# Optimization experiments

Hardware: AMD Instinct MI355X
Metric: run time of the kernel (lower is better)

Reference implementation:

```python
import jax, jax.numpy as jnp
import numpy as np

B, S, DIM, H = 8, 2048, 128, 8
HD = DIM // H  # 16
SCALE = 1.0 / np.sqrt(256.0).astype(np.float32)  # faithful: original divides by sqrt(256)=16


def setup_inputs() -> dict:
    key = jax.random.key(0)
    ks = jax.random.split(key, 8)
    w_std = 1.0 / np.sqrt(DIM).astype(np.float32)
    return {
        "q": jax.random.normal(ks[0], (B, S, DIM), jnp.float32),
        "k": jax.random.normal(ks[1], (B, S, DIM), jnp.float32),
        "v": jax.random.normal(ks[2], (B, S, DIM), jnp.float32),
        "Wq": jax.random.normal(ks[3], (DIM, DIM), jnp.float32) * w_std,
        "bq": jnp.zeros((DIM,), jnp.float32),
        "Wk": jax.random.normal(ks[4], (DIM, DIM), jnp.float32) * w_std,
        "bk": jnp.zeros((DIM,), jnp.float32),
        "Wv": jax.random.normal(ks[5], (DIM, DIM), jnp.float32) * w_std,
        "bv": jnp.zeros((DIM,), jnp.float32),
        "Wo": jax.random.normal(ks[6], (DIM, DIM), jnp.float32) * w_std,
        "bo": jnp.zeros((DIM,), jnp.float32),
    }


def reference(q, k, v, Wq, bq, Wk, bk, Wv, bv, Wo, bo):
    # QKV projections
    Q = q @ Wq + bq  # [B,S,DIM]
    K = k @ Wk + bk
    V = v @ Wv + bv
    # split heads: [B,H,S,HD]
    Q = Q.reshape(B, S, H, HD).transpose(0, 2, 1, 3)
    K = K.reshape(B, S, H, HD).transpose(0, 2, 1, 3)
    V = V.reshape(B, S, H, HD).transpose(0, 2, 1, 3)
    # scaled dot-product attention (note non-standard scale 1/16)
    scores = jnp.einsum("bhqd,bhkd->bhqk", Q, K) * SCALE
    attn = jax.nn.softmax(scores, axis=-1)
    out = jnp.einsum("bhqk,bhkd->bhqd", attn, V)
    out = out.transpose(0, 2, 1, 3).reshape(B, S, DIM)
    return out @ Wo + bo
```

## Files before the change

### kernel.cpp

```cpp
#include <hip/hip_runtime.h>

typedef __attribute__((ext_vector_type(8))) short short8;
typedef __attribute__((ext_vector_type(16))) float f32x16;
typedef _Float16 h8 __attribute__((ext_vector_type(8)));
typedef unsigned int uint;
typedef unsigned short ushort;

#define NS 2048
#define QSCALE 0.0901684400555602f

__device__ __forceinline__ ushort f2h(float f) {
  _Float16 h = (_Float16)f;
  return __builtin_bit_cast(ushort, h);
}
__device__ __forceinline__ uint pkrtz_u(float a, float b) {
  uint r;
  asm("v_cvt_pkrtz_f16_f32 %0, %1, %2" : "=v"(r) : "v"(a), "v"(b));
  return r;
}
__device__ __forceinline__ float fast_exp2(float x) {
#if __has_builtin(__builtin_amdgcn_exp2f)
  return __builtin_amdgcn_exp2f(x);
#else
  return exp2f(x);
#endif
}

__global__ __launch_bounds__(256) void qkv_mfma(
    const float* __restrict__ qin, const float* __restrict__ kin, const float* __restrict__ vin,
    const float* __restrict__ Wq, const float* __restrict__ bq,
    const float* __restrict__ Wk, const float* __restrict__ bk,
    const float* __restrict__ Wv, const float* __restrict__ bv,
    ushort* __restrict__ Qh, ushort* __restrict__ Kh, ushort* __restrict__ Vt) {
  __shared__ __align__(16) ushort Wt[128 * 136];
  __shared__ __align__(16) ushort Al[64 * 136];
  const int tid = threadIdx.x;
  const int p = blockIdx.y;
  const float* A = (p == 0) ? qin : (p == 1) ? kin : vin;
  const float* W = (p == 0) ? Wq : (p == 1) ? Wk : Wv;
  const float* bias = (p == 0) ? bq : (p == 1) ? bk : bv;
  const float wscale = (p == 0) ? QSCALE : 1.0f;
  const int rbase = blockIdx.x * 64;
  {
    const int n = tid & 127, kg = tid >> 7;
#pragma unroll
    for (int k8 = 0; k8 < 8; ++k8) {
      int k0 = k8 * 16 + kg * 8;
      float w[8];
#pragma unroll
      for (int j = 0; j < 8; ++j) w[j] = W[(k0 + j) * 128 + n] * wscale;
      uint4 pk;
      pk.x = pkrtz_u(w[0], w[1]);
      pk.y = pkrtz_u(w[2], w[3]);
      pk.z = pkrtz_u(w[4], w[5]);
      pk.w = pkrtz_u(w[6], w[7]);
      *reinterpret_cast<uint4*>(&Wt[n * 136 + k0]) = pk;
    }
  }
#pragma unroll
  for (int it = 0; it < 8; ++it) {
    int fl = it * 256 + tid;
    int r = fl >> 5, c4 = (fl & 31) << 2;
    float4 a = *reinterpret_cast<const float4*>(A + (size_t)(rbase + r) * 128 + c4);
    uint2 pk;
    pk.x = pkrtz_u(a.x, a.y);
    pk.y = pkrtz_u(a.z, a.w);
    *reinterpret_cast<uint2*>(&Al[r * 136 + c4]) = pk;
  }
  __syncthreads();
  const int lane = tid & 63, wid = tid >> 6;
  const int l31 = lane & 31, hi = lane >> 5;
  const int rh = wid >> 1, ch = wid & 1;
  f32x16 acc[2];
#pragma unroll
  for (int i = 0; i < 2; ++i)
#pragma unroll
    for (int j = 0; j < 16; ++j) acc[i][j] = 0.f;
  const ushort* arow = &Al[(rh * 32 + l31) * 136 + hi * 8];
#pragma unroll
  for (int kk = 0; kk < 8; ++kk) {
    const h8 af = *reinterpret_cast<const h8*>(arow + kk * 16);
#pragma unroll
    for (int i = 0; i < 2; ++i) {
      int nt = ch * 2 + i;
      const h8 bf = *reinterpret_cast<const h8*>(&Wt[(nt * 32 + l31) * 136 + kk * 16 + hi * 8]);
      acc[i] = __builtin_amdgcn_mfma_f32_32x32x16_f16(af, bf, acc[i], 0, 0, 0);
    }
  }
  const int bI = rbase >> 11;
  if (p < 2) {
    ushort* outp = (p == 0) ? Qh : Kh;
#pragma unroll
    for (int i = 0; i < 2; ++i) {
      int c = (ch * 2 + i) * 32 + l31;
      int h = c >> 4, d = c & 15;
      float bb = bias[c] * wscale;
#pragma unroll
      for (int r = 0; r < 16; ++r) {
        int s = rbase + rh * 32 + ((r & 3) + ((r >> 2) << 3) + (hi << 2));
        int sl = s & 2047;
        outp[((size_t)((bI << 3) + h) * 2048 + sl) * 16 + d] = f2h(acc[i][r] + bb);
      }
    }
  } else {
    __syncthreads();
    ushort* CL = Wt;
#pragma unroll
    for (int i = 0; i < 2; ++i) {
      int c = (ch * 2 + i) * 32 + l31;
      float bb = bias[c];
#pragma unroll
      for (int g = 0; g < 4; ++g) {
        uint2 pk;
        pk.x = pkrtz_u(acc[i][g * 4 + 0] + bb, acc[i][g * 4 + 1] + bb);
        pk.y = pkrtz_u(acc[i][g * 4 + 2] + bb, acc[i][g * 4 + 3] + bb);
        int sl0 = rh * 32 + g * 8 + (hi << 2);
        *reinterpret_cast<uint2*>(&CL[c * 72 + sl0]) = pk;
      }
    }
    __syncthreads();
    const int slb = rbase & 2047;
#pragma unroll
    for (int it = 0; it < 4; ++it) {
      int fl = it * 256 + tid;
      int c = fl >> 3, s8 = (fl & 7) * 8;
      short8 val = *reinterpret_cast<const short8*>(&CL[c * 72 + s8]);
      int h = c >> 4, d = c & 15;
      *reinterpret_cast<short8*>(&Vt[((size_t)((bI << 3) + h) * 16 + d) * 2048 + slb + s8]) = val;
    }
  }
}

__global__ __launch_bounds__(256, 4) void attn_kernel(
    const ushort* __restrict__ Qh, const ushort* __restrict__ Kh,
    const ushort* __restrict__ Vtg, ushort* __restrict__ aout) {
  __shared__ __align__(16) ushort Kl[256 * 24];
  __shared__ __align__(16) ushort Vl[17 * 264];
  const int tid = threadIdx.x;
  const int lane = tid & 63, wv = tid >> 6;
  const int l31 = lane & 31, hi = lane >> 5;
  const int bh = blockIdx.x, qt = blockIdx.y;
  for (int e = tid; e < 264; e += 256) Vl[16 * 264 + e] = 0x3C00;
  const int q0 = qt * 128 + wv * 32;
  const h8 qf = *reinterpret_cast<const h8*>(Qh + ((size_t)bh * NS + q0 + l31) * 16 + hi * 8);
  f32x16 oac0, oac1, zc;
#pragma unroll
  for (int i = 0; i < 16; ++i) { oac0[i] = 0.f; oac1[i] = 0.f; zc[i] = 0.f; }
  const int vrow = (l31 < 17) ? l31 : 16;
  const ushort* Kg = Kh + (size_t)bh * NS * 16;
  const ushort* Vg = Vtg + (size_t)bh * 16 * NS;
  const ushort* kbl = &Kl[l31 * 24 + hi * 8];
  const ushort* vbase = &Vl[vrow * 264 + hi * 8];
  const int key0 = tid >> 1, hh = tid & 1, vd = tid >> 5, vc = (tid & 31) * 8;
  const int vgrp = vc & ~31, vk0 = vc & 31;
  const int vs1 = vgrp + ((vk0 & 16) | ((vk0 & 8) >> 1));

  short8 rk0, rk1, rv0, rv1;
#define LOADT(T)                                                                          \
  {                                                                                       \
    int kb = (T) * 256;                                                                   \
    rk0 = *reinterpret_cast<const short8*>(Kg + (size_t)(kb + key0) * 16 + hh * 8);       \
    rk1 = *reinterpret_cast<const short8*>(Kg + (size_t)(kb + 128 + key0) * 16 + hh * 8); \
    rv0 = *reinterpret_cast<const short8*>(Vg + (size_t)vd * NS + kb + vc);               \
    rv1 = *reinterpret_cast<const short8*>(Vg + (size_t)(8 + vd) * NS + kb + vc);         \
  }
#define WRITET()                                                                          \
  {                                                                                       \
    *reinterpret_cast<short8*>(&Kl[key0 * 24 + hh * 8]) = rk0;                            \
    *reinterpret_cast<short8*>(&Kl[(128 + key0) * 24 + hh * 8]) = rk1;                    \
    union { short8 s; uint2 u[2]; } c0, c1;                                               \
    c0.s = rv0; c1.s = rv1;                                                               \
    *reinterpret_cast<uint2*>(&Vl[vd * 264 + vs1]) = c0.u[0];                             \
    *reinterpret_cast<uint2*>(&Vl[vd * 264 + vs1 + 8]) = c0.u[1];                         \
    *reinterpret_cast<uint2*>(&Vl[(8 + vd) * 264 + vs1]) = c1.u[0];                       \
    *reinterpret_cast<uint2*>(&Vl[(8 + vd) * 264 + vs1 + 8]) = c1.u[1];                   \
  }

  LOADT(0);
  WRITET();
  __syncthreads();
  for (int t = 0; t < 8; ++t) {
    if (t < 7) LOADT(t + 1);
#pragma unroll
    for (int kt = 0; kt < 8; ++kt) {
      const h8 kf = *reinterpret_cast<const h8*>(kbl + kt * 768);
      f32x16 sc = __builtin_amdgcn_mfma_f32_32x32x16_f16(kf, qf, zc, 0, 0, 0);
      float pr[16];
#pragma unroll
      for (int r = 0; r < 16; ++r) pr[r] = fast_exp2(sc[r]);
      {
        union { uint u[4]; h8 h; } pf;
        pf.u[0] = pkrtz_u(pr[0], pr[1]);
        pf.u[1] = pkrtz_u(pr[2], pr[3]);
        pf.u[2] = pkrtz_u(pr[4], pr[5]);
        pf.u[3] = pkrtz_u(pr[6], pr[7]);
        const h8 vf = *reinterpret_cast<const h8*>(vbase + kt * 32);
        oac0 = __builtin_amdgcn_mfma_f32_32x32x16_f16(pf.h, vf, oac0, 0, 0, 0);
      }
      {
        union { uint u[4]; h8 h; } pf;
        pf.u[0] = pkrtz_u(pr[8], pr[9]);
        pf.u[1] = pkrtz_u(pr[10], pr[11]);
        pf.u[2] = pkrtz_u(pr[12], pr[13]);
        pf.u[3] = pkrtz_u(pr[14], pr[15]);
        const h8 vf = *reinterpret_cast<const h8*>(vbase + kt * 32 + 16);
        oac1 = __builtin_amdgcn_mfma_f32_32x32x16_f16(pf.h, vf, oac1, 0, 0, 0);
      }
    }
    if (t < 7) {
      __syncthreads();
      WRITET();
      __syncthreads();
    }
  }
#undef LOADT
#undef WRITET
  const int b = bh >> 3, h = bh & 7;
  const int d = l31;
#pragma unroll
  for (int r = 0; r < 16; ++r) {
    float ov = oac0[r] + oac1[r];
    float ls = __shfl(ov, 16 + (hi << 5), 64);
    if (d < 16) {
      int qrow = q0 + ((r & 3) + ((r >> 2) << 3) + (hi << 2));
      aout[((size_t)(b * NS + qrow)) * 128 + h * 16 + d] = f2h(ov / ls);
    }
  }
}

__global__ __launch_bounds__(256) void out_mfma(
    const ushort* __restrict__ Ain, const float* __restrict__ Wo,
    const float* __restrict__ bo, float* __restrict__ out) {
  __shared__ __align__(16) ushort Wt[128 * 136];
  __shared__ __align__(16) ushort Al[32 * 136];
  const int tid = threadIdx.x;
  const int rbase = blockIdx.x * 32;
  {
    const int n = tid & 127, kg = tid >> 7;
#pragma unroll
    for (int k8 = 0; k8 < 8; ++k8) {
      int k0 = k8 * 16 + kg * 8;
      float w[8];
#pragma unroll
      for (int j = 0; j < 8; ++j) w[j] = Wo[(k0 + j) * 128 + n];
      uint4 pk;
      pk.x = pkrtz_u(w[0], w[1]);
      pk.y = pkrtz_u(w[2], w[3]);
      pk.z = pkrtz_u(w[4], w[5]);
      pk.w = pkrtz_u(w[6], w[7]);
      *reinterpret_cast<uint4*>(&Wt[n * 136 + k0]) = pk;
    }
  }
#pragma unroll
  for (int it = 0; it < 2; ++it) {
    int fl = it * 256 + tid;
    int r = fl >> 4, c8 = (fl & 15) * 8;
    *reinterpret_cast<short8*>(&Al[r * 136 + c8]) =
        *reinterpret_cast<const short8*>(Ain + (size_t)(rbase + r) * 128 + c8);
  }
  __syncthreads();
  const int lane = tid & 63, wid = tid >> 6;
  const int l31 = lane & 31, hi = lane >> 5;
  f32x16 acc;
#pragma unroll
  for (int j = 0; j < 16; ++j) acc[j] = 0.f;
  const ushort* arow = &Al[l31 * 136 + hi * 8];
#pragma unroll
  for (int kk = 0; kk < 8; ++kk) {
    const h8 af = *reinterpret_cast<const h8*>(arow + kk * 16);
    const h8 bf = *reinterpret_cast<const h8*>(&Wt[(wid * 32 + l31) * 136 + kk * 16 + hi * 8]);
    acc = __builtin_amdgcn_mfma_f32_32x32x16_f16(af, bf, acc, 0, 0, 0);
  }
  const int c = wid * 32 + l31;
  const float bb = bo[c];
#pragma unroll
  for (int r = 0; r < 16; ++r) {
    int s = rbase + ((r & 3) + ((r >> 2) << 3) + (hi << 2));
    out[(size_t)s * 128 + c] = acc[r] + bb;
  }
}

extern "C" void kernel_launch(void* const* d_in, const int* in_sizes, int n_in,
                              void* d_out, int out_size, void* d_ws, size_t ws_size,
                              hipStream_t stream) {
  const float* q  = (const float*)d_in[0];
  const float* k  = (const float*)d_in[1];
  const float* v  = (const float*)d_in[2];
  const float* Wq = (const float*)d_in[3];
  const float* bq = (const float*)d_in[4];
  const float* Wk = (const float*)d_in[5];
  const float* bk = (const float*)d_in[6];
  const float* Wv = (const float*)d_in[7];
  const float* bv = (const float*)d_in[8];
  const float* Wo = (const float*)d_in[9];
  const float* bo = (const float*)d_in[10];
  float* out = (float*)d_out;

  ushort* Qh = (ushort*)d_out;
  ushort* Kh = Qh + 2097152;
  ushort* Vt = (ushort*)d_ws;
  ushort* aout = Vt + 2097152;

  hipLaunchKernelGGL(qkv_mfma, dim3(256, 3), dim3(256), 0, stream,
                     q, k, v, Wq, bq, Wk, bk, Wv, bv, Qh, Kh, Vt);
  hipLaunchKernelGGL(attn_kernel, dim3(64, 16), dim3(256), 0, stream, Qh, Kh, Vt, aout);
  hipLaunchKernelGGL(out_mfma, dim3(512), dim3(256), 0, stream, aout, Wo, bo, out);
}
```

Baseline: 57.59 us.

## Load K and V fragments directly from global memory, dropping LDS staging

The attention kernel no longer stages K and V tiles through shared memory with double-buffered register prefetch and barriers. Each lane now reads its MFMA operand fragments straight from global memory (relying on L1/L2 caching), and the ones-column used for the softmax denominator is built by a per-lane select instead of an LDS row. This removes the LDS writes and __syncthreads, but global load latency is now exposed inside the compute loop with no explicit prefetch, and the V reads are narrow 8-byte loads.

```diff
diff --git a/kernel.cpp b/kernel.cpp
--- a/kernel.cpp
+++ b/kernel.cpp
@@ -134,87 +134,60 @@
 __global__ __launch_bounds__(256, 4) void attn_kernel(
     const ushort* __restrict__ Qh, const ushort* __restrict__ Kh,
     const ushort* __restrict__ Vtg, ushort* __restrict__ aout) {
-  __shared__ __align__(16) ushort Kl[256 * 24];
-  __shared__ __align__(16) ushort Vl[17 * 264];
   const int tid = threadIdx.x;
   const int lane = tid & 63, wv = tid >> 6;
   const int l31 = lane & 31, hi = lane >> 5;
   const int bh = blockIdx.x, qt = blockIdx.y;
-  for (int e = tid; e < 264; e += 256) Vl[16 * 264 + e] = 0x3C00;
   const int q0 = qt * 128 + wv * 32;
   const h8 qf = *reinterpret_cast<const h8*>(Qh + ((size_t)bh * NS + q0 + l31) * 16 + hi * 8);
   f32x16 oac0, oac1, zc;
 #pragma unroll
   for (int i = 0; i < 16; ++i) { oac0[i] = 0.f; oac1[i] = 0.f; zc[i] = 0.f; }
-  const int vrow = (l31 < 17) ? l31 : 16;
-  const ushort* Kg = Kh + (size_t)bh * NS * 16;
-  const ushort* Vg = Vtg + (size_t)bh * 16 * NS;
-  const ushort* kbl = &Kl[l31 * 24 + hi * 8];
-  const ushort* vbase = &Vl[vrow * 264 + hi * 8];
-  const int key0 = tid >> 1, hh = tid & 1, vd = tid >> 5, vc = (tid & 31) * 8;
-  const int vgrp = vc & ~31, vk0 = vc & 31;
-  const int vs1 = vgrp + ((vk0 & 16) | ((vk0 & 8) >> 1));
-
-  short8 rk0, rk1, rv0, rv1;
-#define LOADT(T)                                                                          \
-  {                                                                                       \
-    int kb = (T) * 256;                                                                   \
-    rk0 = *reinterpret_cast<const short8*>(Kg + (size_t)(kb + key0) * 16 + hh * 8);       \
-    rk1 = *reinterpret_cast<const short8*>(Kg + (size_t)(kb + 128 + key0) * 16 + hh * 8); \
-    rv0 = *reinterpret_cast<const short8*>(Vg + (size_t)vd * NS + kb + vc);               \
-    rv1 = *reinterpret_cast<const short8*>(Vg + (size_t)(8 + vd) * NS + kb + vc);         \
-  }
-#define WRITET()                                                                          \
-  {                                                                                       \
-    *reinterpret_cast<short8*>(&Kl[key0 * 24 + hh * 8]) = rk0;                            \
-    *reinterpret_cast<short8*>(&Kl[(128 + key0) * 24 + hh * 8]) = rk1;                    \
-    union { short8 s; uint2 u[2]; } c0, c1;                                               \
-    c0.s = rv0; c1.s = rv1;                                                               \
-    *reinterpret_cast<uint2*>(&Vl[vd * 264 + vs1]) = c0.u[0];                             \
-    *reinterpret_cast<uint2*>(&Vl[vd * 264 + vs1 + 8]) = c0.u[1];                         \
-    *reinterpret_cast<uint2*>(&Vl[(8 + vd) * 264 + vs1]) = c1.u[0];                       \
-    *reinterpret_cast<uint2*>(&Vl[(8 + vd) * 264 + vs1 + 8]) = c1.u[1];                   \
-  }
-
-  LOADT(0);
-  WRITET();
-  __syncthreads();
-  for (int t = 0; t < 8; ++t) {
-    if (t < 7) LOADT(t + 1);
-#pragma unroll
-    for (int kt = 0; kt < 8; ++kt) {
-      const h8 kf = *reinterpret_cast<const h8*>(kbl + kt * 768);
-      f32x16 sc = __builtin_amdgcn_mfma_f32_32x32x16_f16(kf, qf, zc, 0, 0, 0);
-      float pr[16];
-#pragma unroll
-      for (int r = 0; r < 16; ++r) pr[r] = fast_exp2(sc[r]);
-      {
-        union { uint u[4]; h8 h; } pf;
-        pf.u[0] = pkrtz_u(pr[0], pr[1]);
-        pf.u[1] = pkrtz_u(pr[2], pr[3]);
-        pf.u[2] = pkrtz_u(pr[4], pr[5]);
-        pf.u[3] = pkrtz_u(pr[6], pr[7]);
-        const h8 vf = *reinterpret_cast<const h8*>(vbase + kt * 32);
-        oac0 = __builtin_amdgcn_mfma_f32_32x32x16_f16(pf.h, vf, oac0, 0, 0, 0);
-      }
-      {
-        union { uint u[4]; h8 h; } pf;
-        pf.u[0] = pkrtz_u(pr[8], pr[9]);
-        pf.u[1] = pkrtz_u(pr[10], pr[11]);
-        pf.u[2] = pkrtz_u(pr[12], pr[13]);
-        pf.u[3] = pkrtz_u(pr[14], pr[15]);
-        const h8 vf = *reinterpret_cast<const h8*>(vbase + kt * 32 + 16);
-        oac1 = __builtin_amdgcn_mfma_f32_32x32x16_f16(pf.h, vf, oac1, 0, 0, 0);
-      }
-    }
-    if (t < 7) {
-      __syncthreads();
-      WRITET();
-      __syncthreads();
-    }
-  }
-#undef LOADT
-#undef WRITET
+  const int vrow = (l31 < 16) ? l31 : 0;
+  const bool vones = (l31 >= 16);
+  const uint ONES2 = 0x3C003C00u;
+  const ushort* kp = Kh + (size_t)bh * NS * 16 + l31 * 16 + hi * 8;
+  const ushort* Vr = Vtg + (size_t)bh * 16 * NS + (size_t)vrow * NS + hi * 4;
+
+#pragma unroll 4
+  for (int c = 0; c < 64; ++c) {
+    const int kb = c * 32;
+    const h8 kf = *reinterpret_cast<const h8*>(kp + (size_t)kb * 16);
+    f32x16 sc = __builtin_amdgcn_mfma_f32_32x32x16_f16(kf, qf, zc, 0, 0, 0);
+    float pr[16];
+#pragma unroll
+    for (int r = 0; r < 16; ++r) pr[r] = fast_exp2(sc[r]);
+    {
+      union { uint u[4]; h8 h; } pf;
+      pf.u[0] = pkrtz_u(pr[0], pr[1]);
+      pf.u[1] = pkrtz_u(pr[2], pr[3]);
+      pf.u[2] = pkrtz_u(pr[4], pr[5]);
+      pf.u[3] = pkrtz_u(pr[6], pr[7]);
+      const uint2 va = *reinterpret_cast<const uint2*>(Vr + kb);
+      const uint2 vb = *reinterpret_cast<const uint2*>(Vr + kb + 8);
+      union { uint u[4]; h8 h; } vv;
+      vv.u[0] = vones ? ONES2 : va.x;
+      vv.u[1] = vones ? ONES2 : va.y;
+      vv.u[2] = vones ? ONES2 : vb.x;
+      vv.u[3] = vones ? ONES2 : vb.y;
+      oac0 = __builtin_amdgcn_mfma_f32_32x32x16_f16(pf.h, vv.h, oac0, 0, 0, 0);
+    }
+    {
+      union { uint u[4]; h8 h; } pf;
+      pf.u[0] = pkrtz_u(pr[8], pr[9]);
+      pf.u[1] = pkrtz_u(pr[10], pr[11]);
+      pf.u[2] = pkrtz_u(pr[12], pr[13]);
+      pf.u[3] = pkrtz_u(pr[14], pr[15]);
+      const uint2 va = *reinterpret_cast<const uint2*>(Vr + kb + 16);
+      const uint2 vb = *reinterpret_cast<const uint2*>(Vr + kb + 24);
+      union { uint u[4]; h8 h; } vv;
+      vv.u[0] = vones ? ONES2 : va.x;
+      vv.u[1] = vones ? ONES2 : va.y;
+      vv.u[2] = vones ? ONES2 : vb.x;
+      vv.u[3] = vones ? ONES2 : vb.y;
+      oac1 = __builtin_amdgcn_mfma_f32_32x32x16_f16(pf.h, vv.h, oac1, 0, 0, 0);
+    }
+  }
   const int b = bh >> 3, h = bh & 7;
   const int d = l31;
 #pragma unroll
```

New measurement: 103.5 us. +79.8%, slower.

## Split attention over key range with a separate combine kernel

Applied to the files above, without the earlier changes.

Adds a split-K attention kernel that processes half the keys per block (grid z=2), writing unnormalized fp16 partial outputs and row sums to workspace, plus a combine kernel that adds the partials and normalizes before the output projection. This doubles the number of attention blocks to fill more CUs and shortens each block's serial key loop. In exchange it adds an extra kernel launch and extra global traffic for the partials. It falls back to the original path if the workspace is too small. There is no max subtraction, so the sum of the two partials stays consistent.

```diff
diff --git a/kernel.cpp b/kernel.cpp
--- a/kernel.cpp
+++ b/kernel.cpp
@@ -213,8 +213,6 @@
       __syncthreads();
     }
   }
-#undef LOADT
-#undef WRITET
   const int b = bh >> 3, h = bh & 7;
   const int d = l31;
 #pragma unroll
@@ -226,6 +224,128 @@
       aout[((size_t)(b * NS + qrow)) * 128 + h * 16 + d] = f2h(ov / ls);
     }
   }
+#undef LOADT
+#undef WRITET
+}
+
+__global__ __launch_bounds__(256, 4) void attn_split(
+    const ushort* __restrict__ Qh, const ushort* __restrict__ Kh,
+    const ushort* __restrict__ Vtg, ushort* __restrict__ po, float* __restrict__ ps) {
+  __shared__ __align__(16) ushort Kl[256 * 24];
+  __shared__ __align__(16) ushort Vl[17 * 264];
+  const int tid = threadIdx.x;
+  const int lane = tid & 63, wv = tid >> 6;
+  const int l31 = lane & 31, hi = lane >> 5;
+  const int bh = blockIdx.x, qt = blockIdx.y, split = blockIdx.z;
+  const int koff = split * 1024;
+  for (int e = tid; e < 264; e += 256) Vl[16 * 264 + e] = 0x3C00;
+  const int q0 = qt * 128 + wv * 32;
+  const h8 qf = *reinterpret_cast<const h8*>(Qh + ((size_t)bh * NS + q0 + l31) * 16 + hi * 8);
+  f32x16 oac0, oac1, zc;
+#pragma unroll
+  for (int i = 0; i < 16; ++i) { oac0[i] = 0.f; oac1[i] = 0.f; zc[i] = 0.f; }
+  const int vrow = (l31 < 17) ? l31 : 16;
+  const ushort* Kg = Kh + (size_t)bh * NS * 16;
+  const ushort* Vg = Vtg + (size_t)bh * 16 * NS;
+  const ushort* kbl = &Kl[l31 * 24 + hi * 8];
+  const ushort* vbase = &Vl[vrow * 264 + hi * 8];
+  const int key0 = tid >> 1, hh = tid & 1, vd = tid >> 5, vc = (tid & 31) * 8;
+  const int vgrp = vc & ~31, vk0 = vc & 31;
+  const int vs1 = vgrp + ((vk0 & 16) | ((vk0 & 8) >> 1));
+
+  short8 rk0, rk1, rv0, rv1;
+#define LOADT(T)                                                                          \
+  {                                                                                       \
+    int kb = koff + (T) * 256;                                                            \
+    rk0 = *reinterpret_cast<const short8*>(Kg + (size_t)(kb + key0) * 16 + hh * 8);       \
+    rk1 = *reinterpret_cast<const short8*>(Kg + (size_t)(kb + 128 + key0) * 16 + hh * 8); \
+    rv0 = *reinterpret_cast<const short8*>(Vg + (size_t)vd * NS + kb + vc);               \
+    rv1 = *reinterpret_cast<const short8*>(Vg + (size_t)(8 + vd) * NS + kb + vc);         \
+  }
+#define WRITET()                                                                          \
+  {                                                                                       \
+    *reinterpret_cast<short8*>(&Kl[key0 * 24 + hh * 8]) = rk0;                            \
+    *reinterpret_cast<short8*>(&Kl[(128 + key0) * 24 + hh * 8]) = rk1;                    \
+    union { short8 s; uint2 u[2]; } c0, c1;                                               \
+    c0.s = rv0; c1.s = rv1;                                                               \
+    *reinterpret_cast<uint2*>(&Vl[vd * 264 + vs1]) = c0.u[0];                             \
+    *reinterpret_cast<uint2*>(&Vl[vd * 264 + vs1 + 8]) = c0.u[1];                         \
+    *reinterpret_cast<uint2*>(&Vl[(8 + vd) * 264 + vs1]) = c1.u[0];                       \
+    *reinterpret_cast<uint2*>(&Vl[(8 + vd) * 264 + vs1 + 8]) = c1.u[1];                   \
+  }
+
+  LOADT(0);
+  WRITET();
+  __syncthreads();
+  for (int t = 0; t < 4; ++t) {
+    if (t < 3) LOADT(t + 1);
+#pragma unroll
+    for (int kt = 0; kt < 8; ++kt) {
+      const h8 kf = *reinterpret_cast<const h8*>(kbl + kt * 768);
+      f32x16 sc = __builtin_amdgcn_mfma_f32_32x32x16_f16(kf, qf, zc, 0, 0, 0);
+      float pr[16];
+#pragma unroll
+      for (int r = 0; r < 16; ++r) pr[r] = fast_exp2(sc[r]);
+      {
+        union { uint u[4]; h8 h; } pf;
+        pf.u[0] = pkrtz_u(pr[0], pr[1]);
+        pf.u[1] = pkrtz_u(pr[2], pr[3]);
+        pf.u[2] = pkrtz_u(pr[4], pr[5]);
+        pf.u[3] = pkrtz_u(pr[6], pr[7]);
+        const h8 vf = *reinterpret_cast<const h8*>(vbase + kt * 32);
+        oac0 = __builtin_amdgcn_mfma_f32_32x32x16_f16(pf.h, vf, oac0, 0, 0, 0);
+      }
+      {
+        union { uint u[4]; h8 h; } pf;
+        pf.u[0] = pkrtz_u(pr[8], pr[9]);
+        pf.u[1] = pkrtz_u(pr[10], pr[11]);
+        pf.u[2] = pkrtz_u(pr[12], pr[13]);
+        pf.u[3] = pkrtz_u(pr[14], pr[15]);
+        const h8 vf = *reinterpret_cast<const h8*>(vbase + kt * 32 + 16);
+        oac1 = __builtin_amdgcn_mfma_f32_32x32x16_f16(pf.h, vf, oac1, 0, 0, 0);
+      }
+    }
+    if (t < 3) {
+      __syncthreads();
+      WRITET();
+      __syncthreads();
+    }
+  }
+#undef LOADT
+#undef WRITET
+  const int d = l31;
+  const size_t base = (size_t)(split * 64 + bh) * 2048;
+#pragma unroll
+  for (int r = 0; r < 16; ++r) {
+    float ov = oac0[r] + oac1[r];
+    float ls = __shfl(ov, 16 + (hi << 5), 64);
+    int qrow = q0 + ((r & 3) + ((r >> 2) << 3) + (hi << 2));
+    if (d < 16) po[(base + qrow) * 16 + d] = f2h(ov);
+    if (d == 0) ps[base + qrow] = ls;
+  }
+}
+
+__global__ __launch_bounds__(256) void combine_kernel(
+    const ushort* __restrict__ po, const float* __restrict__ ps,
+    ushort* __restrict__ aout) {
+  const int i8 = blockIdx.x * 256 + threadIdx.x;
+  const int flat = i8 * 8;
+  const int d0 = flat & 15;
+  const int qrow = (flat >> 4) & 2047;
+  const int bh = flat >> 15;
+  const h8 a = *reinterpret_cast<const h8*>(po + flat);
+  const h8 b = *reinterpret_cast<const h8*>(po + 2097152 + flat);
+  const float s = ps[bh * 2048 + qrow] + ps[131072 + bh * 2048 + qrow];
+  const float rinv = 1.0f / s;
+  union { uint u[4]; short8 s8; } o;
+#pragma unroll
+  for (int j = 0; j < 4; ++j) {
+    float v0 = ((float)a[2 * j] + (float)b[2 * j]) * rinv;
+    float v1 = ((float)a[2 * j + 1] + (float)b[2 * j + 1]) * rinv;
+    o.u[j] = pkrtz_u(v0, v1);
+  }
+  const size_t idx = ((size_t)((bh >> 3) * 2048 + qrow)) * 128 + (bh & 7) * 16 + d0;
+  *reinterpret_cast<short8*>(aout + idx) = o.s8;
 }
 
 __global__ __launch_bounds__(256) void out_mfma(
@@ -299,10 +419,21 @@
   ushort* Qh = (ushort*)d_out;
   ushort* Kh = Qh + 2097152;
   ushort* Vt = (ushort*)d_ws;
-  ushort* aout = Vt + 2097152;
 
   hipLaunchKernelGGL(qkv_mfma, dim3(256, 3), dim3(256), 0, stream,
                      q, k, v, Wq, bq, Wk, bk, Wv, bv, Qh, Kh, Vt);
-  hipLaunchKernelGGL(attn_kernel, dim3(64, 16), dim3(256), 0, stream, Qh, Kh, Vt, aout);
-  hipLaunchKernelGGL(out_mfma, dim3(512), dim3(256), 0, stream, aout, Wo, bo, out);
-}
+
+  if (ws_size >= 13631488u) {
+    ushort* po = Vt + 2097152;
+    float* ps = (float*)((char*)d_ws + 12582912);
+    ushort* aout = Vt;
+    hipLaunchKernelGGL(attn_split, dim3(64, 16, 2), dim3(256), 0, stream,
+                       Qh, Kh, Vt, po, ps);
+    hipLaunchKernelGGL(combine_kernel, dim3(1024), dim3(256), 0, stream, po, ps, aout);
+    hipLaunchKernelGGL(out_mfma, dim3(512), dim3(256), 0, stream, aout, Wo, bo, out);
+  } else {
+    ushort* aout = Vt + 2097152;
+    hipLaunchKernelGGL(attn_kernel, dim3(64, 16), dim3(256), 0, stream, Qh, Kh, Vt, aout);
+    hipLaunchKernelGGL(out_mfma, dim3(512), dim3(256), 0, stream, aout, Wo, bo, out);
+  }
+}
```

Measured after the change: 62.34 us. +8.2%, slower.
